# Performance work log

Measured on AMD Instinct MI355X. Metric: run time of the kernel, lower is better.

## Reference

```python
import jax, jax.numpy as jnp
import numpy as np

B, S, H = 2, 2048, 1024
E, I = 8, 4096
TOP_K = 2
W_SCALE = 0.02


def setup_inputs() -> dict:
    key = jax.random.key(0)
    k1, k2, k3, k4, k5 = jax.random.split(key, 5)
    return {
        "hidden_states": jax.random.normal(k1, (B, S, H), dtype=jnp.float32),
        "gate_w": jax.random.normal(k2, (H, E), dtype=jnp.float32) * W_SCALE,
        "w1s": jax.random.normal(k3, (E, H, I), dtype=jnp.float32) * W_SCALE,
        "w2s": jax.random.normal(k4, (E, I, H), dtype=jnp.float32) * W_SCALE,
        "w3s": jax.random.normal(k5, (E, H, I), dtype=jnp.float32) * W_SCALE,
    }


def reference(hidden_states, gate_w, w1s, w2s, w3s):
    b, s, h = hidden_states.shape
    x = hidden_states.reshape(-1, h)                      # [T, H]
    # Router: softmax in fp32, top-k, renormalize (matches torch F.softmax(dtype=float) + topk)
    logits = x @ gate_w                                   # [T, E]
    probs = jax.nn.softmax(logits.astype(jnp.float32), axis=-1)
    rw, sel = jax.lax.top_k(probs, TOP_K)                 # [T, K], [T, K]
    rw = rw / jnp.sum(rw, axis=-1, keepdims=True)
    # Per-token combine weight for each expert: [T, E]
    comb = jnp.sum(jax.nn.one_hot(sel, E, dtype=x.dtype) * rw[..., None].astype(x.dtype), axis=1)
    # Expert SwiGLU MLPs; loop over small fixed expert count (same math as grouped GEMM + scatter)
    out = jnp.zeros_like(x)
    for e in range(E):
        inter = jax.nn.silu(x @ w1s[e]) * (x @ w3s[e])    # [T, I]
        out = out + comb[:, e:e + 1] * (inter @ w2s[e])   # [T, H]
    return out.reshape(b, s, h)
```

## Files before the change

kernel.cpp:

```cpp
#include <hip/hip_runtime.h>

#define T_TOK 4096
#define H_DIM 1024
#define I_DIM 4096
#define NE 8

typedef _Float16 f16;
typedef _Float16 f16x8 __attribute__((ext_vector_type(8)));
typedef _Float16 f16x4 __attribute__((ext_vector_type(4)));
typedef float f32x4 __attribute__((ext_vector_type(4)));

#define GLOBAL_AS __attribute__((address_space(1)))
#define LDS_AS __attribute__((address_space(3)))

__device__ __forceinline__ void gload_lds16(const void* g, void* l) {
  __builtin_amdgcn_global_load_lds((GLOBAL_AS const unsigned int*)g,
                                   (LDS_AS unsigned int*)l, 16, 0, 0);
}

#define VM4() asm volatile("s_waitcnt vmcnt(4)" ::: "memory")
#define VM3() asm volatile("s_waitcnt vmcnt(3)" ::: "memory")
#define VM0() asm volatile("s_waitcnt vmcnt(0)" ::: "memory")
#define BAR() __builtin_amdgcn_s_barrier()
#define PRIO1() __builtin_amdgcn_s_setprio(1)
#define PRIO0() __builtin_amdgcn_s_setprio(0)

__global__ void cast_x_kernel(const float* __restrict__ x, f16* __restrict__ xh) {
  int i = blockIdx.x * 256 + threadIdx.x;
  float4 v = reinterpret_cast<const float4*>(x)[i];
  f16x4 o = {(f16)v.x, (f16)v.y, (f16)v.z, (f16)v.w};
  reinterpret_cast<f16x4*>(xh)[i] = o;
}

__global__ __launch_bounds__(256) void transpose_cast_kernel(
    const float* __restrict__ w1s, const float* __restrict__ w3s,
    const float* __restrict__ w2s, f16* __restrict__ w13t, f16* __restrict__ w2t) {
  __shared__ float tile[64][65];
  const int z = blockIdx.z;
  const int tr = threadIdx.x >> 4;
  const int tc = (threadIdx.x & 15) * 4;
  if (z < 16) {
    int e = z & 7;
    const float* in = (z < 8 ? w1s : w3s) + (size_t)e * H_DIM * I_DIM;
    f16* out = w13t + (size_t)e * (2 * H_DIM * I_DIM);
    const int roff = (z < 8) ? 0 : 32;
    const int c0 = blockIdx.x * 64, r0 = blockIdx.y * 64;
#pragma unroll
    for (int i = 0; i < 4; ++i) {
      int r = tr + i * 16;
      float4 v = *reinterpret_cast<const float4*>(&in[(size_t)(r0 + r) * I_DIM + c0 + tc]);
      tile[r][tc] = v.x; tile[r][tc + 1] = v.y; tile[r][tc + 2] = v.z; tile[r][tc + 3] = v.w;
    }
    __syncthreads();
#pragma unroll
    for (int i = 0; i < 4; ++i) {
      int oc = tr + i * 16;
      int cg = c0 + oc;
      int rowo = ((cg >> 5) << 6) + roff + (cg & 31);
      f16x4 h;
#pragma unroll
      for (int j = 0; j < 4; ++j) h[j] = (f16)tile[tc + j][oc];
      *reinterpret_cast<f16x4*>(&out[(size_t)rowo * H_DIM + r0 + tc]) = h;
    }
  } else {
    int e = z - 16;
    const float* in = w2s + (size_t)e * H_DIM * I_DIM;
    f16* out = w2t + (size_t)e * H_DIM * I_DIM;
    const int r0 = blockIdx.x * 64, c0 = blockIdx.y * 64;
#pragma unroll
    for (int i = 0; i < 4; ++i) {
      int r = tr + i * 16;
      float4 v = *reinterpret_cast<const float4*>(&in[(size_t)(r0 + r) * H_DIM + c0 + tc]);
      tile[r][tc] = v.x; tile[r][tc + 1] = v.y; tile[r][tc + 2] = v.z; tile[r][tc + 3] = v.w;
    }
    __syncthreads();
#pragma unroll
    for (int i = 0; i < 4; ++i) {
      int oc = tr + i * 16;
      f16x4 h;
#pragma unroll
      for (int j = 0; j < 4; ++j) h[j] = (f16)tile[tc + j][oc];
      *reinterpret_cast<f16x4*>(&out[(size_t)(c0 + oc) * I_DIM + r0 + tc]) = h;
    }
  }
}

__global__ void router_kernel(const float* __restrict__ x, const float* __restrict__ gw,
                              int* __restrict__ counts, int* __restrict__ lists,
                              float* __restrict__ wgts) {
  const int t = blockIdx.x;
  const int l = threadIdx.x;
  const float* xr = x + (size_t)t * H_DIM;
  float acc[NE];
#pragma unroll
  for (int e = 0; e < NE; ++e) acc[e] = 0.f;
  for (int k = l; k < H_DIM; k += 64) {
    float xv = xr[k];
#pragma unroll
    for (int e = 0; e < NE; ++e) acc[e] += xv * gw[k * NE + e];
  }
#pragma unroll
  for (int e = 0; e < NE; ++e) {
    float v = acc[e];
#pragma unroll
    for (int off = 32; off > 0; off >>= 1) v += __shfl_xor(v, off);
    acc[e] = v;
  }
  if (l == 0) {
    int i1 = 0;
#pragma unroll
    for (int e = 1; e < NE; ++e)
      if (acc[e] > acc[i1]) i1 = e;
    int i2 = (i1 == 0) ? 1 : 0;
#pragma unroll
    for (int e = 0; e < NE; ++e)
      if (e != i1 && acc[e] > acc[i2]) i2 = e;
    float wA = 1.f / (1.f + __expf(acc[i2] - acc[i1]));
    float wB = 1.f - wA;
    int p1 = atomicAdd(&counts[i1], 1);
    lists[i1 * T_TOK + p1] = t;
    wgts[i1 * T_TOK + p1] = wA;
    int p2 = atomicAdd(&counts[i2], 1);
    lists[i2 * T_TOK + p2] = t;
    wgts[i2 * T_TOK + p2] = wB;
  }
}

__global__ void prefix_kernel(const int* __restrict__ counts, int* __restrict__ bases) {
  if (threadIdx.x == 0) {
    int s = 0;
#pragma unroll
    for (int e = 0; e < NE; ++e) {
      bases[e] = s;
      s += (counts[e] + 127) & ~127;
    }
  }
}

__global__ __launch_bounds__(512, 1) void gemm_a_kernel(
    const f16* __restrict__ xh, const f16* __restrict__ w13t,
    const int* __restrict__ counts, const int* __restrict__ bases,
    const int* __restrict__ lists, f16* __restrict__ inter) {
  const int z = blockIdx.z;
  const int cnt = counts[z];
  const int r0 = blockIdx.y * 256;
  if (r0 >= cnt) return;
  const int base = bases[z];
  const int pad = (cnt + 127) & ~127;
  const int c0 = blockIdx.x * 256;
  const int tid = threadIdx.x;
  const int lane = tid & 63;
  const int wid = tid >> 6;
  const int wm = wid >> 2, wn = wid & 3;
  const int lrow = lane & 15, lk = lane >> 4;

  __shared__ __align__(16) f16 lds[2][32768];

  const int* lst = lists + z * T_TOK;
  const f16* w13 = w13t + (size_t)z * (2 * H_DIM * I_DIM);

  const int srow = tid >> 1;
  const int gb = (tid & 1) ^ ((srow >> 2) & 1);
  const int tok = lst[r0 + srow];
  const f16* asrc = xh + (size_t)tok * H_DIM + gb * 8;
  const f16* bsrc = w13 + (size_t)(c0 + srow) * H_DIM + gb * 8;

#define STG_A(r, S, K) gload_lds16(asrc + (K) + (r) * 16, &lds[S][((r) * 512 + wid * 64) * 8])
#define STG_B(r, S, K) gload_lds16(bsrc + (K) + (r) * 16, &lds[S][16384 + ((r) * 512 + wid * 64) * 8])

  const f32x4 z4 = {0.f, 0.f, 0.f, 0.f};
  f32x4 acc[8][4];
#pragma unroll
  for (int m = 0; m < 8; ++m)
#pragma unroll
    for (int n = 0; n < 4; ++n) acc[m][n] = z4;

  const int NT = H_DIM / 64;
  STG_A(0, 0, 0); STG_A(1, 0, 0); STG_B(0, 0, 0); STG_B(1, 0, 0);
  STG_A(2, 0, 0); STG_A(3, 0, 0); STG_B(2, 0, 0); STG_B(3, 0, 0);
  VM4(); BAR();

  int cur = 0;
  for (int t = 0; t < NT; ++t) {
    const f16* SA = lds[cur];
    const f16* SB = lds[cur] + 16384;
    const int nxt = cur ^ 1;
    const int ks = (t + 1 < NT ? t + 1 : NT - 1) * 64;

#pragma unroll
    for (int kk = 0; kk < 2; ++kk) {
      if (kk == 0) { STG_A(0, nxt, ks); STG_A(1, nxt, ks); }
      else         { STG_A(2, nxt, ks); STG_A(3, nxt, ks); }
      f16x8 af[8];
#pragma unroll
      for (int m = 0; m < 8; ++m) {
        int row = wm * 128 + m * 16 + lrow;
        int idx = ((kk * 2 + (lk >> 1)) * 512 + row * 2 + ((lk & 1) ^ ((row >> 2) & 1))) * 8;
        af[m] = *reinterpret_cast<const f16x8*>(&SA[idx]);
      }
#pragma unroll
      for (int nh = 0; nh < 2; ++nh) {
        if (nh == 1) {
          if (kk == 0) { STG_B(0, nxt, ks); STG_B(1, nxt, ks); }
          else         { STG_B(2, nxt, ks); STG_B(3, nxt, ks); }
        }
        f16x8 bf[2];
#pragma unroll
        for (int n = 0; n < 2; ++n) {
          int row = wn * 64 + (nh * 2 + n) * 16 + lrow;
          int idx = ((kk * 2 + (lk >> 1)) * 512 + row * 2 + ((lk & 1) ^ ((row >> 2) & 1))) * 8;
          bf[n] = *reinterpret_cast<const f16x8*>(&SB[idx]);
        }
        PRIO1();
#pragma unroll
        for (int m = 0; m < 8; ++m)
#pragma unroll
          for (int n = 0; n < 2; ++n)
            acc[m][nh * 2 + n] =
                __builtin_amdgcn_mfma_f32_16x16x32_f16(af[m], bf[n], acc[m][nh * 2 + n], 0, 0, 0);
        PRIO0();
      }
      VM4(); BAR();
    }
    cur ^= 1;
  }
  VM0();
#undef STG_A
#undef STG_B

#pragma unroll
  for (int m = 0; m < 8; ++m)
#pragma unroll
    for (int r = 0; r < 4; ++r) {
      int rowl = wm * 128 + m * 16 + lk * 4 + r;
      if (r0 + rowl < pad) {
        size_t grow = base + r0 + rowl;
#pragma unroll
        for (int n = 0; n < 2; ++n) {
          int col = (c0 >> 1) + wn * 32 + n * 16 + lrow;
          float s1 = acc[m][n][r];
          float s3 = acc[m][n + 2][r];
          float sv = s1 / (1.f + __expf(-s1));
          inter[grow * I_DIM + col] = (f16)(sv * s3);
        }
      }
    }
}

__global__ __launch_bounds__(512, 1) void gemm_b_kernel(
    const f16* __restrict__ inter, const f16* __restrict__ w2t,
    const int* __restrict__ counts, const int* __restrict__ bases,
    const int* __restrict__ lists, const float* __restrict__ wgts,
    float* __restrict__ out) {
  const int z = blockIdx.z;
  const int cnt = counts[z];
  const int r0 = blockIdx.y * 128;
  if (r0 >= cnt) return;
  const int base = bases[z];
  const int c0 = blockIdx.x * 256;
  const int tid = threadIdx.x;
  const int lane = tid & 63;
  const int wid = tid >> 6;
  const int wm = wid >> 2, wn = wid & 3;
  const int lrow = lane & 15, lk = lane >> 4;

  __shared__ __align__(16) f16 lds[2][24576];

  const int* lst = lists + z * T_TOK;
  const float* wgt = wgts + z * T_TOK;
  const f16* w2 = w2t + (size_t)z * I_DIM * H_DIM;

  const int rowA = (tid & 255) >> 1;
  const int gbA = (tid & 1) ^ ((rowA >> 2) & 1);
  const f16* asrc = inter + (size_t)(base + r0 + rowA) * I_DIM + ((tid >> 8) & 1) * 16 + gbA * 8;
  const int rowB = tid >> 1;
  const int gbB = (tid & 1) ^ ((rowB >> 2) & 1);
  const f16* bsrc = w2 + (size_t)(c0 + rowB) * I_DIM + gbB * 8;

#define STG_A(r, S, K) gload_lds16(asrc + (K) + (r) * 32, &lds[S][((r) * 512 + wid * 64) * 8])
#define STG_B(r, S, K) gload_lds16(bsrc + (K) + (r) * 16, &lds[S][8192 + ((r) * 512 + wid * 64) * 8])

  const f32x4 z4 = {0.f, 0.f, 0.f, 0.f};
  f32x4 acc[4][4];
#pragma unroll
  for (int m = 0; m < 4; ++m)
#pragma unroll
    for (int n = 0; n < 4; ++n) acc[m][n] = z4;

  const int NT = I_DIM / 64;
  STG_A(0, 0, 0); STG_B(0, 0, 0); STG_B(1, 0, 0);
  STG_A(1, 0, 0); STG_B(2, 0, 0); STG_B(3, 0, 0);
  VM3(); BAR();

  int cur = 0;
  for (int t = 0; t < NT; ++t) {
    const f16* SA = lds[cur];
    const f16* SB = lds[cur] + 8192;
    const int nxt = cur ^ 1;
    const int ks = (t + 1 < NT ? t + 1 : NT - 1) * 64;

#pragma unroll
    for (int kk = 0; kk < 2; ++kk) {
      if (kk == 0) { STG_A(0, nxt, ks); STG_B(0, nxt, ks); }
      else         { STG_A(1, nxt, ks); STG_B(2, nxt, ks); }
      f16x8 af[4];
#pragma unroll
      for (int m = 0; m < 4; ++m) {
        int row = wm * 64 + m * 16 + lrow;
        int idx = ((kk * 2 + (lk >> 1)) * 256 + row * 2 + ((lk & 1) ^ ((row >> 2) & 1))) * 8;
        af[m] = *reinterpret_cast<const f16x8*>(&SA[idx]);
      }
#pragma unroll
      for (int nh = 0; nh < 2; ++nh) {
        if (nh == 1) { if (kk == 0) STG_B(1, nxt, ks); else STG_B(3, nxt, ks); }
        f16x8 bf[2];
#pragma unroll
        for (int n = 0; n < 2; ++n) {
          int row = wn * 64 + (nh * 2 + n) * 16 + lrow;
          int idx = ((kk * 2 + (lk >> 1)) * 512 + row * 2 + ((lk & 1) ^ ((row >> 2) & 1))) * 8;
          bf[n] = *reinterpret_cast<const f16x8*>(&SB[idx]);
        }
        PRIO1();
#pragma unroll
        for (int m = 0; m < 4; ++m)
#pragma unroll
          for (int n = 0; n < 2; ++n)
            acc[m][nh * 2 + n] =
                __builtin_amdgcn_mfma_f32_16x16x32_f16(af[m], bf[n], acc[m][nh * 2 + n], 0, 0, 0);
        PRIO0();
      }
      VM3(); BAR();
    }
    cur ^= 1;
  }
  VM0();
#undef STG_A
#undef STG_B

#pragma unroll
  for (int m = 0; m < 4; ++m)
#pragma unroll
    for (int r = 0; r < 4; ++r) {
      int ri = r0 + wm * 64 + m * 16 + lk * 4 + r;
      if (ri < cnt) {
        int tok = lst[ri];
        float wg = wgt[ri];
        float* orow = out + (size_t)tok * H_DIM + c0 + wn * 64 + lrow;
#pragma unroll
        for (int n = 0; n < 4; ++n) atomicAdd(&orow[n * 16], wg * acc[m][n][r]);
      }
    }
}

extern "C" void kernel_launch(void* const* d_in, const int* in_sizes, int n_in,
                              void* d_out, int out_size, void* d_ws, size_t ws_size,
                              hipStream_t stream) {
  const float* x = (const float*)d_in[0];
  const float* gw = (const float*)d_in[1];
  const float* w1s = (const float*)d_in[2];
  const float* w2s = (const float*)d_in[3];
  const float* w3s = (const float*)d_in[4];
  float* out = (float*)d_out;

  char* ws = (char*)d_ws;
  f16* xh = (f16*)ws;
  f16* inter = (f16*)(ws + ((size_t)8 << 20));
  f16* w13t = (f16*)(ws + ((size_t)80 << 20));
  f16* w2t = (f16*)(ws + ((size_t)208 << 20));
  char* meta = ws + ((size_t)272 << 20);
  int* counts = (int*)meta;
  int* bases = (int*)(meta + 512);
  int* lists = (int*)(meta + 1024);
  float* wgts = (float*)(meta + 1024 + (size_t)NE * T_TOK * 4);

  hipMemsetAsync(out, 0, (size_t)out_size * sizeof(float), stream);
  hipMemsetAsync(meta, 0, 1024 + (size_t)NE * T_TOK * 8, stream);

  cast_x_kernel<<<dim3((T_TOK * H_DIM) / (4 * 256)), dim3(256), 0, stream>>>(x, xh);
  router_kernel<<<dim3(T_TOK), dim3(64), 0, stream>>>(x, gw, counts, lists, wgts);
  prefix_kernel<<<dim3(1), dim3(64), 0, stream>>>(counts, bases);
  transpose_cast_kernel<<<dim3(64, 16, 24), dim3(256), 0, stream>>>(
      w1s, w3s, w2s, w13t, w2t);
  gemm_a_kernel<<<dim3((2 * I_DIM) / 256, T_TOK / 256, NE), dim3(512), 0, stream>>>(
      xh, w13t, counts, bases, lists, inter);
  gemm_b_kernel<<<dim3(H_DIM / 256, T_TOK / 128, NE), dim3(512), 0, stream>>>(
      inter, w2t, counts, bases, lists, wgts, out);
}
```

Before: 608.3 us.

## Use triple-buffered LDS ring with BK=32 and split-K in expert GEMMs

Both expert GEMMs switch from a double-buffered 64-wide K tile to a three-slot LDS ring of 32-wide K tiles, prefetching two stages ahead with a new XOR swizzle. The smaller LDS footprint lets each kernel request two blocks per CU. The down-projection kernel moves to 256 threads with 256x128 tiles and a two-way split-K whose partial sums combine through the existing atomic adds. The aim is better latency hiding and occupancy, at the cost of more atomic traffic on the output and possible register pressure from 128 fp32 accumulators per thread at two blocks per CU.

```diff
diff --git a/kernel.cpp b/kernel.cpp
--- a/kernel.cpp
+++ b/kernel.cpp
@@ -4,6 +4,7 @@
 #define H_DIM 1024
 #define I_DIM 4096
 #define NE 8
+#define INTER_ROWS 9216
 
 typedef _Float16 f16;
 typedef _Float16 f16x8 __attribute__((ext_vector_type(8)));
@@ -18,8 +19,8 @@
                                    (LDS_AS unsigned int*)l, 16, 0, 0);
 }
 
+#define VM6() asm volatile("s_waitcnt vmcnt(6)" ::: "memory")
 #define VM4() asm volatile("s_waitcnt vmcnt(4)" ::: "memory")
-#define VM3() asm volatile("s_waitcnt vmcnt(3)" ::: "memory")
 #define VM0() asm volatile("s_waitcnt vmcnt(0)" ::: "memory")
 #define BAR() __builtin_amdgcn_s_barrier()
 #define PRIO1() __builtin_amdgcn_s_setprio(1)
@@ -137,7 +138,7 @@
   }
 }
 
-__global__ __launch_bounds__(512, 1) void gemm_a_kernel(
+__global__ __launch_bounds__(512, 2) void gemm_a_kernel(
     const f16* __restrict__ xh, const f16* __restrict__ w13t,
     const int* __restrict__ counts, const int* __restrict__ bases,
     const int* __restrict__ lists, f16* __restrict__ inter) {
@@ -154,19 +155,29 @@
   const int wm = wid >> 2, wn = wid & 3;
   const int lrow = lane & 15, lk = lane >> 4;
 
-  __shared__ __align__(16) f16 lds[2][32768];
+  __shared__ __align__(16) f16 ring[3][16384];
 
   const int* lst = lists + z * T_TOK;
   const f16* w13 = w13t + (size_t)z * (2 * H_DIM * I_DIM);
 
-  const int srow = tid >> 1;
-  const int gb = (tid & 1) ^ ((srow >> 2) & 1);
-  const int tok = lst[r0 + srow];
-  const f16* asrc = xh + (size_t)tok * H_DIM + gb * 8;
-  const f16* bsrc = w13 + (size_t)(c0 + srow) * H_DIM + gb * 8;
-
-#define STG_A(r, S, K) gload_lds16(asrc + (K) + (r) * 16, &lds[S][((r) * 512 + wid * 64) * 8])
-#define STG_B(r, S, K) gload_lds16(bsrc + (K) + (r) * 16, &lds[S][16384 + ((r) * 512 + wid * 64) * 8])
+  const f16 *asrc[2], *bsrc[2];
+#pragma unroll
+  for (int i = 0; i < 2; ++i) {
+    int sf = i * 512 + tid;
+    int row = sf >> 2;
+    int sl = (sf & 3) ^ ((row >> 1) & 3);
+    int tok = lst[r0 + row];
+    asrc[i] = xh + (size_t)tok * H_DIM + sl * 8;
+    bsrc[i] = w13 + (size_t)(c0 + row) * H_DIM + sl * 8;
+  }
+
+#define STG(S, K)                                                     \
+  do {                                                                \
+    _Pragma("unroll") for (int i_ = 0; i_ < 2; ++i_)                  \
+      gload_lds16(asrc[i_] + (K), (S) + (i_ * 512 + wid * 64) * 8);   \
+    _Pragma("unroll") for (int i_ = 0; i_ < 2; ++i_)                  \
+      gload_lds16(bsrc[i_] + (K), (S) + 8192 + (i_ * 512 + wid * 64) * 8); \
+  } while (0)
 
   const f32x4 z4 = {0.f, 0.f, 0.f, 0.f};
   f32x4 acc[8][4];
@@ -175,58 +186,38 @@
 #pragma unroll
     for (int n = 0; n < 4; ++n) acc[m][n] = z4;
 
-  const int NT = H_DIM / 64;
-  STG_A(0, 0, 0); STG_A(1, 0, 0); STG_B(0, 0, 0); STG_B(1, 0, 0);
-  STG_A(2, 0, 0); STG_A(3, 0, 0); STG_B(2, 0, 0); STG_B(3, 0, 0);
-  VM4(); BAR();
-
-  int cur = 0;
+  f16 *s0 = ring[0], *s1 = ring[1], *s2 = ring[2];
+  const int NT = H_DIM / 32;
+  STG(s0, 0);
+  STG(s1, 32);
+  VM4();
+  BAR();
+
   for (int t = 0; t < NT; ++t) {
-    const f16* SA = lds[cur];
-    const f16* SB = lds[cur] + 16384;
-    const int nxt = cur ^ 1;
-    const int ks = (t + 1 < NT ? t + 1 : NT - 1) * 64;
-
-#pragma unroll
-    for (int kk = 0; kk < 2; ++kk) {
-      if (kk == 0) { STG_A(0, nxt, ks); STG_A(1, nxt, ks); }
-      else         { STG_A(2, nxt, ks); STG_A(3, nxt, ks); }
-      f16x8 af[8];
-#pragma unroll
-      for (int m = 0; m < 8; ++m) {
-        int row = wm * 128 + m * 16 + lrow;
-        int idx = ((kk * 2 + (lk >> 1)) * 512 + row * 2 + ((lk & 1) ^ ((row >> 2) & 1))) * 8;
-        af[m] = *reinterpret_cast<const f16x8*>(&SA[idx]);
-      }
-#pragma unroll
-      for (int nh = 0; nh < 2; ++nh) {
-        if (nh == 1) {
-          if (kk == 0) { STG_B(0, nxt, ks); STG_B(1, nxt, ks); }
-          else         { STG_B(2, nxt, ks); STG_B(3, nxt, ks); }
-        }
-        f16x8 bf[2];
-#pragma unroll
-        for (int n = 0; n < 2; ++n) {
-          int row = wn * 64 + (nh * 2 + n) * 16 + lrow;
-          int idx = ((kk * 2 + (lk >> 1)) * 512 + row * 2 + ((lk & 1) ^ ((row >> 2) & 1))) * 8;
-          bf[n] = *reinterpret_cast<const f16x8*>(&SB[idx]);
-        }
-        PRIO1();
-#pragma unroll
-        for (int m = 0; m < 8; ++m)
-#pragma unroll
-          for (int n = 0; n < 2; ++n)
-            acc[m][nh * 2 + n] =
-                __builtin_amdgcn_mfma_f32_16x16x32_f16(af[m], bf[n], acc[m][nh * 2 + n], 0, 0, 0);
-        PRIO0();
-      }
-      VM4(); BAR();
-    }
-    cur ^= 1;
-  }
-  VM0();
-#undef STG_A
-#undef STG_B
+    if (t + 2 < NT) STG(s2, (t + 2) * 32);
+    f16x8 af[8], bf[4];
+#pragma unroll
+    for (int m = 0; m < 8; ++m) {
+      int row = wm * 128 + m * 16 + lrow;
+      af[m] = *reinterpret_cast<const f16x8*>(&s0[(row * 4 + (lk ^ ((row >> 1) & 3))) * 8]);
+    }
+#pragma unroll
+    for (int n = 0; n < 4; ++n) {
+      int row = wn * 64 + n * 16 + lrow;
+      bf[n] = *reinterpret_cast<const f16x8*>(&s0[8192 + (row * 4 + (lk ^ ((row >> 1) & 3))) * 8]);
+    }
+    PRIO1();
+#pragma unroll
+    for (int m = 0; m < 8; ++m)
+#pragma unroll
+      for (int n = 0; n < 4; ++n)
+        acc[m][n] = __builtin_amdgcn_mfma_f32_16x16x32_f16(af[m], bf[n], acc[m][n], 0, 0, 0);
+    PRIO0();
+    if (t + 2 < NT) VM4(); else VM0();
+    BAR();
+    f16* tmp = s0; s0 = s1; s1 = s2; s2 = tmp;
+  }
+#undef STG
 
 #pragma unroll
   for (int m = 0; m < 8; ++m)
@@ -238,110 +229,112 @@
 #pragma unroll
         for (int n = 0; n < 2; ++n) {
           int col = (c0 >> 1) + wn * 32 + n * 16 + lrow;
-          float s1 = acc[m][n][r];
-          float s3 = acc[m][n + 2][r];
-          float sv = s1 / (1.f + __expf(-s1));
-          inter[grow * I_DIM + col] = (f16)(sv * s3);
+          float v1 = acc[m][n][r];
+          float v3 = acc[m][n + 2][r];
+          float sv = v1 / (1.f + __expf(-v1));
+          inter[grow * I_DIM + col] = (f16)(sv * v3);
         }
       }
     }
 }
 
-__global__ __launch_bounds__(512, 1) void gemm_b_kernel(
+__global__ __launch_bounds__(256, 2) void gemm_b_kernel(
     const f16* __restrict__ inter, const f16* __restrict__ w2t,
     const int* __restrict__ counts, const int* __restrict__ bases,
     const int* __restrict__ lists, const float* __restrict__ wgts,
     float* __restrict__ out) {
   const int z = blockIdx.z;
   const int cnt = counts[z];
-  const int r0 = blockIdx.y * 128;
+  const int rb = blockIdx.y >> 1, kb = blockIdx.y & 1;
+  const int r0 = rb * 256;
   if (r0 >= cnt) return;
   const int base = bases[z];
-  const int c0 = blockIdx.x * 256;
+  const int c0 = blockIdx.x * 128;
   const int tid = threadIdx.x;
   const int lane = tid & 63;
   const int wid = tid >> 6;
-  const int wm = wid >> 2, wn = wid & 3;
+  const int wm = wid >> 1, wn = wid & 1;
   const int lrow = lane & 15, lk = lane >> 4;
 
-  __shared__ __align__(16) f16 lds[2][24576];
+  __shared__ __align__(16) f16 ring[3][12288];
 
   const int* lst = lists + z * T_TOK;
   const float* wgt = wgts + z * T_TOK;
   const f16* w2 = w2t + (size_t)z * I_DIM * H_DIM;
-
-  const int rowA = (tid & 255) >> 1;
-  const int gbA = (tid & 1) ^ ((rowA >> 2) & 1);
-  const f16* asrc = inter + (size_t)(base + r0 + rowA) * I_DIM + ((tid >> 8) & 1) * 16 + gbA * 8;
-  const int rowB = tid >> 1;
-  const int gbB = (tid & 1) ^ ((rowB >> 2) & 1);
-  const f16* bsrc = w2 + (size_t)(c0 + rowB) * I_DIM + gbB * 8;
-
-#define STG_A(r, S, K) gload_lds16(asrc + (K) + (r) * 32, &lds[S][((r) * 512 + wid * 64) * 8])
-#define STG_B(r, S, K) gload_lds16(bsrc + (K) + (r) * 16, &lds[S][8192 + ((r) * 512 + wid * 64) * 8])
+  const int k0 = kb * 2048;
+
+  const f16* asrc[4];
+#pragma unroll
+  for (int i = 0; i < 4; ++i) {
+    int sf = i * 256 + tid;
+    int row = sf >> 2;
+    int sl = (sf & 3) ^ ((row >> 1) & 3);
+    int gr = base + r0 + row;
+    if (gr > INTER_ROWS - 1) gr = INTER_ROWS - 1;
+    asrc[i] = inter + (size_t)gr * I_DIM + k0 + sl * 8;
+  }
+  const f16* bsrc[2];
+#pragma unroll
+  for (int i = 0; i < 2; ++i) {
+    int sf = i * 256 + tid;
+    int row = sf >> 2;
+    int sl = (sf & 3) ^ ((row >> 1) & 3);
+    bsrc[i] = w2 + (size_t)(c0 + row) * I_DIM + k0 + sl * 8;
+  }
+
+#define STG(S, K)                                                     \
+  do {                                                                \
+    _Pragma("unroll") for (int i_ = 0; i_ < 4; ++i_)                  \
+      gload_lds16(asrc[i_] + (K), (S) + (i_ * 256 + wid * 64) * 8);   \
+    _Pragma("unroll") for (int i_ = 0; i_ < 2; ++i_)                  \
+      gload_lds16(bsrc[i_] + (K), (S) + 8192 + (i_ * 256 + wid * 64) * 8); \
+  } while (0)
 
   const f32x4 z4 = {0.f, 0.f, 0.f, 0.f};
-  f32x4 acc[4][4];
-#pragma unroll
-  for (int m = 0; m < 4; ++m)
+  f32x4 acc[8][4];
+#pragma unroll
+  for (int m = 0; m < 8; ++m)
 #pragma unroll
     for (int n = 0; n < 4; ++n) acc[m][n] = z4;
 
-  const int NT = I_DIM / 64;
-  STG_A(0, 0, 0); STG_B(0, 0, 0); STG_B(1, 0, 0);
-  STG_A(1, 0, 0); STG_B(2, 0, 0); STG_B(3, 0, 0);
-  VM3(); BAR();
-
-  int cur = 0;
+  f16 *s0 = ring[0], *s1 = ring[1], *s2 = ring[2];
+  const int NT = 2048 / 32;
+  STG(s0, 0);
+  STG(s1, 32);
+  VM6();
+  BAR();
+
   for (int t = 0; t < NT; ++t) {
-    const f16* SA = lds[cur];
-    const f16* SB = lds[cur] + 8192;
-    const int nxt = cur ^ 1;
-    const int ks = (t + 1 < NT ? t + 1 : NT - 1) * 64;
-
-#pragma unroll
-    for (int kk = 0; kk < 2; ++kk) {
-      if (kk == 0) { STG_A(0, nxt, ks); STG_B(0, nxt, ks); }
-      else         { STG_A(1, nxt, ks); STG_B(2, nxt, ks); }
-      f16x8 af[4];
-#pragma unroll
-      for (int m = 0; m < 4; ++m) {
-        int row = wm * 64 + m * 16 + lrow;
-        int idx = ((kk * 2 + (lk >> 1)) * 256 + row * 2 + ((lk & 1) ^ ((row >> 2) & 1))) * 8;
-        af[m] = *reinterpret_cast<const f16x8*>(&SA[idx]);
-      }
-#pragma unroll
-      for (int nh = 0; nh < 2; ++nh) {
-        if (nh == 1) { if (kk == 0) STG_B(1, nxt, ks); else STG_B(3, nxt, ks); }
-        f16x8 bf[2];
-#pragma unroll
-        for (int n = 0; n < 2; ++n) {
-          int row = wn * 64 + (nh * 2 + n) * 16 + lrow;
-          int idx = ((kk * 2 + (lk >> 1)) * 512 + row * 2 + ((lk & 1) ^ ((row >> 2) & 1))) * 8;
-          bf[n] = *reinterpret_cast<const f16x8*>(&SB[idx]);
-        }
-        PRIO1();
-#pragma unroll
-        for (int m = 0; m < 4; ++m)
-#pragma unroll
-          for (int n = 0; n < 2; ++n)
-            acc[m][nh * 2 + n] =
-                __builtin_amdgcn_mfma_f32_16x16x32_f16(af[m], bf[n], acc[m][nh * 2 + n], 0, 0, 0);
-        PRIO0();
-      }
-      VM3(); BAR();
-    }
-    cur ^= 1;
-  }
-  VM0();
-#undef STG_A
-#undef STG_B
-
-#pragma unroll
-  for (int m = 0; m < 4; ++m)
+    if (t + 2 < NT) STG(s2, (t + 2) * 32);
+    f16x8 af[8], bf[4];
+#pragma unroll
+    for (int m = 0; m < 8; ++m) {
+      int row = wm * 128 + m * 16 + lrow;
+      af[m] = *reinterpret_cast<const f16x8*>(&s0[(row * 4 + (lk ^ ((row >> 1) & 3))) * 8]);
+    }
+#pragma unroll
+    for (int n = 0; n < 4; ++n) {
+      int row = wn * 64 + n * 16 + lrow;
+      bf[n] = *reinterpret_cast<const f16x8*>(&s0[8192 + (row * 4 + (lk ^ ((row >> 1) & 3))) * 8]);
+    }
+    PRIO1();
+#pragma unroll
+    for (int m = 0; m < 8; ++m)
+#pragma unroll
+      for (int n = 0; n < 4; ++n)
+        acc[m][n] = __builtin_amdgcn_mfma_f32_16x16x32_f16(af[m], bf[n], acc[m][n], 0, 0, 0);
+    PRIO0();
+    if (t + 2 < NT) VM6(); else VM0();
+    BAR();
+    f16* tmp = s0; s0 = s1; s1 = s2; s2 = tmp;
+  }
+#undef STG
+
+#pragma unroll
+  for (int m = 0; m < 8; ++m)
 #pragma unroll
     for (int r = 0; r < 4; ++r) {
-      int ri = r0 + wm * 64 + m * 16 + lk * 4 + r;
+      int ri = r0 + wm * 128 + m * 16 + lk * 4 + r;
       if (ri < cnt) {
         int tok = lst[ri];
         float wg = wgt[ri];
@@ -383,6 +376,6 @@
       w1s, w3s, w2s, w13t, w2t);
   gemm_a_kernel<<<dim3((2 * I_DIM) / 256, T_TOK / 256, NE), dim3(512), 0, stream>>>(
       xh, w13t, counts, bases, lists, inter);
-  gemm_b_kernel<<<dim3(H_DIM / 256, T_TOK / 128, NE), dim3(512), 0, stream>>>(
+  gemm_b_kernel<<<dim3(H_DIM / 128, 2 * (T_TOK / 256), NE), dim3(256), 0, stream>>>(
       inter, w2t, counts, bases, lists, wgts, out);
 }
```

Measured after the change: 566.1 us. 1.07x faster.
